# Kernel optimization log

Measured on AMD Instinct MI355X. Metric: run time of the kernel, lower is better.

Reference implementation:

```python
import jax, jax.numpy as jnp
import numpy as np


def _ln(x, g, b, eps=1e-5):
    m = x.mean(-1, keepdims=True)
    v = ((x - m) ** 2).mean(-1, keepdims=True)
    return g * (x - m) / jnp.sqrt(v + eps) + b


def _mha(x, w_qkv, b_qkv, w_o, b_o, nh):
    B, S, d = x.shape
    hd = d // nh
    qkv = x @ w_qkv.T + b_qkv
    q, k, v = jnp.split(qkv, 3, axis=-1)
    sp = lambda t: t.reshape(B, S, nh, hd).transpose(0, 2, 1, 3)
    q, k, v = sp(q), sp(k), sp(v)
    a = jax.nn.softmax(jnp.einsum('bhqd,bhkd->bhqk', q, k) / np.float32(np.sqrt(hd)), axis=-1)
    o = jnp.einsum('bhqk,bhkd->bhqd', a, v).transpose(0, 2, 1, 3).reshape(B, S, d)
    return o @ w_o.T + b_o


def _enc(x, w_qkv, b_qkv, w_o, b_o, ga, ba, wf1, bf1, wf2, bf2, gb, bb, nh=2):
    # torch TransformerEncoderLayer, post-norm, ReLU FFN
    x = _ln(x + _mha(x, w_qkv, b_qkv, w_o, b_o, nh), ga, ba)
    ff = jax.nn.relu(x @ wf1.T + bf1) @ wf2.T + bf2
    return _ln(x + ff, gb, bb)


def forward(nodes, w_qkv1, b_qkv1, w_o1, b_o1, g1a, bb1a, w_ff1a, bf1a, w_ff1b, bf1b, g1b, bb1b,
            wq, bq, wk, bk, wv, bv, g_co, bb_co, w4, b4, w5, b5, w6, b6,
            w_rel, w_root, b_rgcn, wg_rel, wg_root, bg,
            w_qkv2, b_qkv2, w_o2, b_o2, g2a, bb2a, w_ff2a, bf2a, w_ff2b, bf2b, g2b, bb2b,
            w_l1, b_l1, w_l2, b_l2, edge_index, opt_idx):
    N, H = nodes.shape
    O = 4
    B = opt_idx.shape[0] // O
    # option-node mutual attention (encoder_layer1) + scatter back
    opts = nodes[opt_idx].reshape(B, O, H)
    opts = _enc(opts, w_qkv1, b_qkv1, w_o1, b_o1, g1a, bb1a, w_ff1a, bf1a, w_ff1b, bf1b, g1b, bb1b)
    nodes2 = nodes.at[opt_idx].set(opts.reshape(B * O, H))
    src, dst = edge_index[0], edge_index[1]
    xs, xd = nodes2[src], nodes2[dst]  # [E,H]
    # per-edge 4-head co-attention: node1/node2 are single rows so qk^T is a scalar per head
    hd = H // 4
    q = (xs @ wq.T + bq).reshape(-1, 4, hd)
    k = (xd @ wk.T + bk).reshape(-1, 4, hd)
    v = (xd @ wv.T + bv).reshape(-1, 4, hd)
    s = jnp.einsum('ehd,ehd->eh', q, k) / np.float32(np.sqrt(hd))
    r = (s[..., None] * v).reshape(-1, H)
    co = jax.nn.relu(_ln(r, g_co, bb_co))
    h = jax.nn.relu(co @ w4.T + b4)
    h = jax.nn.relu(h @ w5.T + b5)
    logits = h @ w6.T + b6  # [E,8]
    # original applies Softmax(dim=0) to a [1,8] tensor -> all ones -> argmax picks class 0
    probs = jax.nn.softmax(logits[:, None, :], axis=1)[:, 0, :]
    edge_type = jnp.argmax(probs, axis=-1)
    # RGCNConv(H, H, num_relations=8), mean aggregation per relation + root + bias
    agg = jnp.zeros((N, H), nodes.dtype)
    for rel in range(8):
        m = edge_type == rel
        msg = jnp.where(m[:, None], xs @ w_rel[rel], 0.0)
        ssum = jax.ops.segment_sum(msg, dst, num_segments=N)
        cnt = jax.ops.segment_sum(m.astype(nodes.dtype), dst, num_segments=N)
        agg = agg + ssum / jnp.maximum(cnt, 1.0)[:, None]
    out1 = nodes2 @ w_root + b_rgcn + agg
    # GraphConv(H, 64): add-aggregated neighbors through lin_rel + root through lin_root
    agg2 = jax.ops.segment_sum(out1[src], dst, num_segments=N)
    out2 = agg2 @ wg_rel + bg + out1 @ wg_root  # [N,64]
    # readout over option nodes (encoder_layer2 + tanh(linear1) + linear2)
    opt2 = out2[opt_idx].reshape(B, O, 64)
    opt2 = _enc(opt2, w_qkv2, b_qkv2, w_o2, b_o2, g2a, bb2a, w_ff2a, bf2a, w_ff2b, bf2b, g2b, bb2b)
    opt2 = jnp.tanh(opt2 @ w_l1.T + b_l1)
    return opt2 @ w_l2.T + b_l2  # [B,O,1]


def setup_inputs() -> dict:
    key = jax.random.key(0)
    N, E, B, O, H, F = 20000, 40000, 64, 4, 768, 2048
    ks = iter(jax.random.split(key, 64))
    W = lambda *s: jax.random.normal(next(ks), s, jnp.float32) * 0.02
    return dict(
        nodes=jax.random.normal(next(ks), (N, H), jnp.float32),
        edge_index=jax.random.randint(next(ks), (2, E), 0, N),
        opt_idx=jnp.arange(B * O),
        w_qkv1=W(3 * H, H), b_qkv1=jnp.zeros(3 * H), w_o1=W(H, H), b_o1=jnp.zeros(H),
        g1a=jnp.ones(H), bb1a=jnp.zeros(H),
        w_ff1a=W(F, H), bf1a=jnp.zeros(F), w_ff1b=W(H, F), bf1b=jnp.zeros(H),
        g1b=jnp.ones(H), bb1b=jnp.zeros(H),
        wq=W(H, H), bq=jnp.zeros(H), wk=W(H, H), bk=jnp.zeros(H), wv=W(H, H), bv=jnp.zeros(H),
        g_co=jnp.ones(H), bb_co=jnp.zeros(H),
        w4=W(H, H), b4=jnp.zeros(H), w5=W(64, H), b5=jnp.zeros(64), w6=W(8, 64), b6=jnp.zeros(8),
        w_rel=W(8, H, H), w_root=W(H, H), b_rgcn=jnp.zeros(H),
        wg_rel=W(H, 64), wg_root=W(H, 64), bg=jnp.zeros(64),
        w_qkv2=W(192, 64), b_qkv2=jnp.zeros(192), w_o2=W(64, 64), b_o2=jnp.zeros(64),
        g2a=jnp.ones(64), bb2a=jnp.zeros(64),
        w_ff2a=W(F, 64), bf2a=jnp.zeros(F), w_ff2b=W(64, F), bf2b=jnp.zeros(64),
        g2b=jnp.ones(64), bb2b=jnp.zeros(64),
        w_l1=W(64, 64), b_l1=jnp.zeros(64), w_l2=W(1, 64), b_l2=jnp.zeros(1),
    )


def reference(nodes, edge_index, opt_idx, w_qkv1, b_qkv1, w_o1, b_o1, g1a, bb1a, w_ff1a, bf1a,
              w_ff1b, bf1b, g1b, bb1b, wq, bq, wk, bk, wv, bv, g_co, bb_co, w4, b4, w5, b5, w6, b6,
              w_rel, w_root, b_rgcn, wg_rel, wg_root, bg, w_qkv2, b_qkv2, w_o2, b_o2, g2a, bb2a,
              w_ff2a, bf2a, w_ff2b, bf2b, g2b, bb2b, w_l1, b_l1, w_l2, b_l2):
    return forward(nodes, w_qkv1, b_qkv1, w_o1, b_o1, g1a, bb1a, w_ff1a, bf1a, w_ff1b, bf1b, g1b,
                   bb1b, wq, bq, wk, bk, wv, bv, g_co, bb_co, w4, b4, w5, b5, w6, b6, w_rel, w_root,
                   b_rgcn, wg_rel, wg_root, bg, w_qkv2, b_qkv2, w_o2, b_o2, g2a, bb2a, w_ff2a, bf2a,
                   w_ff2b, bf2b, g2b, bb2b, w_l1, b_l1, w_l2, b_l2, edge_index, opt_idx)
```

## Files before the change

### kernel.cpp

```cpp
#include <hip/hip_runtime.h>

typedef unsigned short u16;
typedef unsigned int u32;
typedef __bf16 bf16x8 __attribute__((ext_vector_type(8)));
typedef float f32x4 __attribute__((ext_vector_type(4)));

__device__ __forceinline__ u16 f2bf(float f) {
    union { float f; u32 u; } v; v.f = f;
    u32 r = v.u + 0x7FFFu + ((v.u >> 16) & 1u);
    return (u16)(r >> 16);
}
__device__ __forceinline__ float bf2f(u16 h) {
    union { u32 u; float f; } v; v.u = (u32)h << 16; return v.f;
}

__global__ __launch_bounds__(256) void gemm_bt(
    const u16* __restrict__ A, const u16* __restrict__ Bt,
    float* __restrict__ C, u16* __restrict__ Cb, const float* __restrict__ bias,
    int M, int N, int K, int relu)
{
    __shared__ char lA[128 * 64 * 2];
    __shared__ char lB[128 * 64 * 2];
    const int t = threadIdx.x;
    const int w = t >> 6, l = t & 63;
    const int bn = blockIdx.x, bm = blockIdx.y;
    const int wr = w >> 1, wc = w & 1;

    const int srow = w * 8 + (l >> 3);
    const int scol = ((l & 7) ^ (l >> 3)) << 3;
    const u16* gA = A + (size_t)(bm * 128 + srow) * K + scol;
    const u16* gB = Bt + (size_t)(bn * 128 + srow) * K + scol;

    f32x4 zero = {0.f, 0.f, 0.f, 0.f};
    f32x4 acc[4][4];
#pragma unroll
    for (int i = 0; i < 4; i++)
#pragma unroll
        for (int j = 0; j < 4; j++) acc[i][j] = zero;

    const int arow = wr * 64 + (l & 15);
    const int brow = wc * 64 + (l & 15);
    const int kx = l >> 4;
    const int sw = l & 7;

    for (int k0 = 0; k0 < K; k0 += 64) {
#pragma unroll
        for (int c2 = 0; c2 < 4; ++c2) {
            __builtin_amdgcn_global_load_lds(
                (const __attribute__((address_space(1))) void*)(gA + (size_t)c2 * 32 * K + k0),
                (__attribute__((address_space(3))) void*)(lA + c2 * 4096 + w * 1024), 16, 0, 0);
            __builtin_amdgcn_global_load_lds(
                (const __attribute__((address_space(1))) void*)(gB + (size_t)c2 * 32 * K + k0),
                (__attribute__((address_space(3))) void*)(lB + c2 * 4096 + w * 1024), 16, 0, 0);
        }
        __syncthreads();
#pragma unroll
        for (int kk = 0; kk < 2; ++kk) {
            bf16x8 af[4], bfr[4];
#pragma unroll
            for (int mi = 0; mi < 4; ++mi)
                af[mi] = *(const bf16x8*)(lA + (arow + mi * 16) * 128 + (((kk * 4 + kx) ^ sw) << 4));
#pragma unroll
            for (int ni = 0; ni < 4; ++ni)
                bfr[ni] = *(const bf16x8*)(lB + (brow + ni * 16) * 128 + (((kk * 4 + kx) ^ sw) << 4));
#pragma unroll
            for (int mi = 0; mi < 4; ++mi)
#pragma unroll
                for (int ni = 0; ni < 4; ++ni)
                    acc[mi][ni] = __builtin_amdgcn_mfma_f32_16x16x32_bf16(af[mi], bfr[ni], acc[mi][ni], 0, 0, 0);
        }
        __syncthreads();
    }

    const int cm = bm * 128 + wr * 64;
    const int cn = bn * 128 + wc * 64;
#pragma unroll
    for (int mi = 0; mi < 4; ++mi) {
#pragma unroll
        for (int ni = 0; ni < 4; ++ni) {
            int row0 = cm + mi * 16 + (l >> 4) * 4;
            int col = cn + ni * 16 + (l & 15);
            float bv = bias ? bias[col] : 0.f;
#pragma unroll
            for (int r = 0; r < 4; ++r) {
                float v = acc[mi][ni][r] + bv;
                if (relu) v = fmaxf(v, 0.f);
                if (Cb) Cb[(size_t)(row0 + r) * N + col] = f2bf(v);
                else    C [(size_t)(row0 + r) * N + col] = v;
            }
        }
    }
}

__global__ __launch_bounds__(256) void gemm_bt_sk(
    const u16* __restrict__ A, const u16* __restrict__ Bt,
    float* __restrict__ P, int M, int N, int K, int Kc)
{
    __shared__ char lA[128 * 64 * 2];
    __shared__ char lB[128 * 64 * 2];
    const int t = threadIdx.x;
    const int w = t >> 6, l = t & 63;
    const int bn = blockIdx.x, bm = blockIdx.y, ks = blockIdx.z;
    const int wr = w >> 1, wc = w & 1;

    const int srow = w * 8 + (l >> 3);
    const int scol = ((l & 7) ^ (l >> 3)) << 3;
    const u16* gA = A + (size_t)(bm * 128 + srow) * K + scol;
    const u16* gB = Bt + (size_t)(bn * 128 + srow) * K + scol;

    f32x4 zero = {0.f, 0.f, 0.f, 0.f};
    f32x4 acc[4][4];
#pragma unroll
    for (int i = 0; i < 4; i++)
#pragma unroll
        for (int j = 0; j < 4; j++) acc[i][j] = zero;

    const int arow = wr * 64 + (l & 15);
    const int brow = wc * 64 + (l & 15);
    const int kx = l >> 4;
    const int sw = l & 7;

    const int kbeg = ks * Kc, kend = kbeg + Kc;
    for (int k0 = kbeg; k0 < kend; k0 += 64) {
#pragma unroll
        for (int c2 = 0; c2 < 4; ++c2) {
            __builtin_amdgcn_global_load_lds(
                (const __attribute__((address_space(1))) void*)(gA + (size_t)c2 * 32 * K + k0),
                (__attribute__((address_space(3))) void*)(lA + c2 * 4096 + w * 1024), 16, 0, 0);
            __builtin_amdgcn_global_load_lds(
                (const __attribute__((address_space(1))) void*)(gB + (size_t)c2 * 32 * K + k0),
                (__attribute__((address_space(3))) void*)(lB + c2 * 4096 + w * 1024), 16, 0, 0);
        }
        __syncthreads();
#pragma unroll
        for (int kk = 0; kk < 2; ++kk) {
            bf16x8 af[4], bfr[4];
#pragma unroll
            for (int mi = 0; mi < 4; ++mi)
                af[mi] = *(const bf16x8*)(lA + (arow + mi * 16) * 128 + (((kk * 4 + kx) ^ sw) << 4));
#pragma unroll
            for (int ni = 0; ni < 4; ++ni)
                bfr[ni] = *(const bf16x8*)(lB + (brow + ni * 16) * 128 + (((kk * 4 + kx) ^ sw) << 4));
#pragma unroll
            for (int mi = 0; mi < 4; ++mi)
#pragma unroll
                for (int ni = 0; ni < 4; ++ni)
                    acc[mi][ni] = __builtin_amdgcn_mfma_f32_16x16x32_bf16(af[mi], bfr[ni], acc[mi][ni], 0, 0, 0);
        }
        __syncthreads();
    }

    float* Pp = P + (size_t)ks * M * N;
    const int cm = bm * 128 + wr * 64;
    const int cn = bn * 128 + wc * 64;
#pragma unroll
    for (int mi = 0; mi < 4; ++mi) {
#pragma unroll
        for (int ni = 0; ni < 4; ++ni) {
            int row0 = cm + mi * 16 + (l >> 4) * 4;
            int col = cn + ni * 16 + (l & 15);
#pragma unroll
            for (int r = 0; r < 4; ++r)
                Pp[(size_t)(row0 + r) * N + col] = acc[mi][ni][r];
        }
    }
}

__global__ void sk_reduce_b(const float* __restrict__ P, int KS, long MN, int N,
                            const float* __restrict__ bias, int relu, u16* __restrict__ outb)
{
    long i = (long)blockIdx.x * blockDim.x + threadIdx.x;
    long stride = (long)gridDim.x * blockDim.x;
    for (; i < MN; i += stride) {
        float v = bias ? bias[i % N] : 0.f;
        for (int ks = 0; ks < KS; ks++) v += P[(size_t)ks * MN + i];
        if (relu) v = fmaxf(v, 0.f);
        outb[i] = f2bf(v);
    }
}

struct CJob { const float* src; u16* dst; long n4; };
struct CJobs6 { CJob j[6]; };
__global__ void conv6_bf16(CJobs6 jobs)
{
    CJob jb = jobs.j[blockIdx.z];
    long i = (long)blockIdx.x * blockDim.x + threadIdx.x;
    long stride = (long)gridDim.x * blockDim.x;
    for (; i < jb.n4; i += stride) {
        float4 v = ((const float4*)jb.src)[i];
        ushort4 o;
        o.x = f2bf(v.x); o.y = f2bf(v.y); o.z = f2bf(v.z); o.w = f2bf(v.w);
        ((ushort4*)jb.dst)[i] = o;
    }
}

struct TJob { const float* src; u16* dst; int Rr, Cc, ldo; };
struct TJobs2 { TJob j[2]; };
__global__ void transpose2_bf16(TJobs2 jobs)
{
    TJob jb = jobs.j[blockIdx.z];
    __shared__ float tile[32][33];
    int c0 = blockIdx.x * 32, r0 = blockIdx.y * 32;
    if (c0 >= jb.Cc || r0 >= jb.Rr) return;
    int tx = threadIdx.x, ty = threadIdx.y;
    for (int dy = 0; dy < 32; dy += 8) {
        int r = r0 + ty + dy, c = c0 + tx;
        tile[ty + dy][tx] = (r < jb.Rr && c < jb.Cc) ? jb.src[(size_t)r * jb.Cc + c] : 0.f;
    }
    __syncthreads();
    for (int dy = 0; dy < 32; dy += 8) {
        int c = c0 + ty + dy, r = r0 + tx;
        if (c < jb.Cc && r < jb.Rr) jb.dst[(size_t)c * jb.ldo + r] = f2bf(tile[tx][ty + dy]);
    }
}

__global__ void bc_prep(const float* __restrict__ b_rgcn, const float* __restrict__ wg_rel,
                        const float* __restrict__ wg_root, float* __restrict__ bc)
{
    int n = threadIdx.x;
    const float* W = (n < 64) ? (wg_rel + n) : (wg_root + (n - 64));
    float s = 0.f;
    for (int k = 0; k < 768; k++) s += b_rgcn[k] * W[(size_t)k * 64];
    bc[n] = s;
}

__global__ void conv_nodes_str(const float* __restrict__ nodes, u16* __restrict__ Abig,
                               int Nn, int Mpad)
{
    long i = (long)blockIdx.x * blockDim.x + threadIdx.x;
    long stride = (long)gridDim.x * blockDim.x;
    long n4 = (long)Mpad * 192;
    for (; i < n4; i += stride) {
        long row = i / 192, c4 = i % 192;
        ushort4 o;
        if ((int)row < Nn) {
            float4 v = ((const float4*)nodes)[i];
            o.x = f2bf(v.x); o.y = f2bf(v.y); o.z = f2bf(v.z); o.w = f2bf(v.w);
        } else { o.x = 0; o.y = 0; o.z = 0; o.w = 0; }
        ((ushort4*)Abig)[row * 384 + c4] = o;
    }
}

__global__ void gather_x0(const float* __restrict__ nodes, const int* __restrict__ opt,
                          float* __restrict__ x0, u16* __restrict__ x0b, int H)
{
    int r = blockIdx.x;
    size_t srcb = (size_t)opt[r] * H;
    for (int c = threadIdx.x; c < H; c += blockDim.x) {
        float v = nodes[srcb + c];
        x0[(size_t)r * H + c] = v;
        x0b[(size_t)r * H + c] = f2bf(v);
    }
}

__global__ __launch_bounds__(256) void attn_fused(
    const float* __restrict__ Pq, int KS, const float* __restrict__ b_qkv1,
    u16* __restrict__ atnob)
{
    __shared__ float Q[4][384], Kk[4][384], V[4][384];
    int b = blockIdx.x >> 1, h = blockIdx.x & 1;
    int w = threadIdx.x >> 6, l = threadIdx.x & 63;
    int row = b * 4 + w;
    const int hb = h * 384;
#pragma unroll
    for (int j = 0; j < 6; j++) {
        int c = hb + j * 64 + l;
        float q = b_qkv1[c], k = b_qkv1[768 + c], v = b_qkv1[1536 + c];
        for (int ks = 0; ks < KS; ks++) {
            const float* Pr = Pq + (size_t)ks * 256 * 2304 + (size_t)row * 2304;
            q += Pr[c]; k += Pr[768 + c]; v += Pr[1536 + c];
        }
        Q[w][j * 64 + l] = q; Kk[w][j * 64 + l] = k; V[w][j * 64 + l] = v;
    }
    __syncthreads();
    float sc[4];
#pragma unroll
    for (int sj = 0; sj < 4; sj++) {
        float p = 0.f;
#pragma unroll
        for (int j = 0; j < 6; j++) p += Q[w][j * 64 + l] * Kk[sj][j * 64 + l];
        for (int off = 32; off; off >>= 1) p += __shfl_down(p, off, 64);
        sc[sj] = __shfl(p, 0, 64) * 0.05103103630798287f;
    }
    float mx = fmaxf(fmaxf(sc[0], sc[1]), fmaxf(sc[2], sc[3]));
    float e0 = __expf(sc[0] - mx), e1 = __expf(sc[1] - mx);
    float e2 = __expf(sc[2] - mx), e3 = __expf(sc[3] - mx);
    float inv = 1.f / (e0 + e1 + e2 + e3);
    e0 *= inv; e1 *= inv; e2 *= inv; e3 *= inv;
#pragma unroll
    for (int j = 0; j < 6; j++) {
        int c = j * 64 + l;
        float o = e0 * V[0][c] + e1 * V[1][c] + e2 * V[2][c] + e3 * V[3][c];
        atnob[(size_t)row * 768 + hb + c] = f2bf(o);
    }
}

__global__ __launch_bounds__(256) void ln_reduce768(
    const float* __restrict__ P, int KS, const float* __restrict__ bias,
    const float* __restrict__ res, const float* __restrict__ g, const float* __restrict__ be,
    float* __restrict__ outf, u16* __restrict__ outb, const int* __restrict__ opt, int ldo)
{
    int r = blockIdx.x, t = threadIdx.x;
    float v[3]; float s = 0.f, q = 0.f;
#pragma unroll
    for (int i = 0; i < 3; i++) {
        int c = t + i * 256;
        float a = bias[c] + res[(size_t)r * 768 + c];
        for (int ks = 0; ks < KS; ks++) a += P[(size_t)ks * 256 * 768 + (size_t)r * 768 + c];
        v[i] = a; s += a; q += a * a;
    }
    for (int off = 32; off; off >>= 1) { s += __shfl_down(s, off, 64); q += __shfl_down(q, off, 64); }
    __shared__ float ss[4], qq[4];
    int w = t >> 6, l = t & 63;
    if (l == 0) { ss[w] = s; qq[w] = q; }
    __syncthreads();
    s = ss[0] + ss[1] + ss[2] + ss[3];
    q = qq[0] + qq[1] + qq[2] + qq[3];
    float m = s * (1.f / 768.f);
    float ri = rsqrtf(q * (1.f / 768.f) - m * m + 1e-5f);
    size_t ob = opt ? (size_t)opt[r] * ldo : (size_t)r * ldo;
#pragma unroll
    for (int i = 0; i < 3; i++) {
        int c = t + i * 256;
        float o = g[c] * (v[i] - m) * ri + be[c];
        if (outf) outf[(size_t)r * 768 + c] = o;
        if (outb) outb[ob + c] = f2bf(o);
    }
}

__global__ void edge_count(const int* __restrict__ ei, int* __restrict__ cnt, int E)
{
    int e = blockIdx.x * blockDim.x + threadIdx.x;
    if (e < E) atomicAdd(&cnt[ei[E + e]], 1);
}

__global__ __launch_bounds__(1024) void scan_offsets(
    const int* __restrict__ cnt, int* __restrict__ offs, int* __restrict__ cur, int n)
{
    __shared__ int part[1024];
    int t = threadIdx.x;
    int per = (n + 1023) / 1024;
    int base = t * per;
    int local = 0;
    for (int i = 0; i < per; i++) {
        int idx = base + i;
        if (idx < n) local += cnt[idx];
    }
    part[t] = local;
    __syncthreads();
    for (int off = 1; off < 1024; off <<= 1) {
        int v = (t >= off) ? part[t - off] : 0;
        __syncthreads();
        part[t] += v;
        __syncthreads();
    }
    int prefix = (t == 0) ? 0 : part[t - 1];
    for (int i = 0; i < per; i++) {
        int idx = base + i;
        if (idx < n) {
            offs[idx] = prefix;
            cur[idx] = prefix;
            prefix += cnt[idx];
        }
    }
}

__global__ void fill_edges(const int* __restrict__ ei, int* __restrict__ cur,
                           int* __restrict__ elist, int E)
{
    int e = blockIdx.x * blockDim.x + threadIdx.x;
    if (e < E) {
        int d = ei[E + e];
        int pos = atomicAdd(&cur[d], 1);
        elist[pos] = ei[e];
    }
}

__global__ __launch_bounds__(256) void gather_mean(
    const int* __restrict__ offs, const int* __restrict__ cnt, const int* __restrict__ elist,
    u16* Abig, int Nn, int Mpad)
{
    int w = threadIdx.x >> 6, l = threadIdx.x & 63;
    int d = blockIdx.x * 4 + w;
    if (d >= Mpad) return;
    float acc[12];
#pragma unroll
    for (int j = 0; j < 12; j++) acc[j] = 0.f;
    float inv = 0.f;
    if (d < Nn) {
        int base = offs[d], c = cnt[d];
        for (int i = 0; i < c; i++) {
            int s = elist[base + i];
            const ushort4* p = (const ushort4*)(Abig + (size_t)s * 1536);
#pragma unroll
            for (int j4 = 0; j4 < 3; j4++) {
                ushort4 v = p[j4 * 64 + l];
                acc[j4 * 4 + 0] += bf2f(v.x);
                acc[j4 * 4 + 1] += bf2f(v.y);
                acc[j4 * 4 + 2] += bf2f(v.z);
                acc[j4 * 4 + 3] += bf2f(v.w);
            }
        }
        inv = 1.f / (float)max(c, 1);
    }
    ushort4* q = (ushort4*)(Abig + (size_t)d * 1536 + 768);
#pragma unroll
    for (int j4 = 0; j4 < 3; j4++) {
        ushort4 o;
        o.x = f2bf(acc[j4 * 4 + 0] * inv);
        o.y = f2bf(acc[j4 * 4 + 1] * inv);
        o.z = f2bf(acc[j4 * 4 + 2] * inv);
        o.w = f2bf(acc[j4 * 4 + 3] * inv);
        q[j4 * 64 + l] = o;
    }
}

__global__ __launch_bounds__(256) void enc2_head(
    const int* __restrict__ opt, const int* __restrict__ offs, const int* __restrict__ cnt,
    const int* __restrict__ elist, const float* __restrict__ C2, const float* __restrict__ bg,
    const float* __restrict__ w_qkv2, const float* __restrict__ b_qkv2,
    const float* __restrict__ w_o2, const float* __restrict__ b_o2,
    const float* __restrict__ g2a, const float* __restrict__ bb2a,
    float* __restrict__ x21)
{
    __shared__ float X[4][64];
    __shared__ float QKV[4][192];
    __shared__ float T[4][64];
    int b = blockIdx.x;
    int w = threadIdx.x >> 6, l = threadIdx.x & 63;
    int row = b * 4 + w;

    {
        int d = opt[row];
        float acc = bg[l] + C2[(size_t)d * 128 + 64 + l];
        int base = offs[d], c = cnt[d];
        for (int i = 0; i < c; i++) {
            int s = elist[base + i];
            acc += C2[(size_t)s * 128 + l];
        }
        X[w][l] = acc;
    }
    __syncthreads();

#pragma unroll
    for (int j = 0; j < 3; j++) {
        int n = l + j * 64;
        const float* wr = w_qkv2 + (size_t)n * 64;
        float s = b_qkv2[n];
        for (int k = 0; k < 64; k++) s += X[w][k] * wr[k];
        QKV[w][n] = s;
    }
    __syncthreads();

    {
        float q = QKV[w][l];
        float p0 = q * QKV[0][64 + l], p1 = q * QKV[1][64 + l];
        float p2 = q * QKV[2][64 + l], p3 = q * QKV[3][64 + l];
#pragma unroll
        for (int off = 1; off < 32; off <<= 1) {
            p0 += __shfl_xor(p0, off, 64); p1 += __shfl_xor(p1, off, 64);
            p2 += __shfl_xor(p2, off, 64); p3 += __shfl_xor(p3, off, 64);
        }
        p0 *= 0.1767766953f; p1 *= 0.1767766953f; p2 *= 0.1767766953f; p3 *= 0.1767766953f;
        float mx = fmaxf(fmaxf(p0, p1), fmaxf(p2, p3));
        float e0 = __expf(p0 - mx), e1 = __expf(p1 - mx), e2 = __expf(p2 - mx), e3 = __expf(p3 - mx);
        float inv = 1.f / (e0 + e1 + e2 + e3);
        T[w][l] = (e0 * QKV[0][128 + l] + e1 * QKV[1][128 + l] +
                   e2 * QKV[2][128 + l] + e3 * QKV[3][128 + l]) * inv;
    }
    __syncthreads();

    {
        const float* wr = w_o2 + (size_t)l * 64;
        float s = b_o2[l];
        for (int k = 0; k < 64; k++) s += T[w][k] * wr[k];
        float xa = s + X[w][l];
        float sum = xa, sq = xa * xa;
#pragma unroll
        for (int off = 1; off < 64; off <<= 1) {
            sum += __shfl_xor(sum, off, 64);
            sq  += __shfl_xor(sq, off, 64);
        }
        float m = sum * (1.f / 64.f);
        float ri = rsqrtf(sq * (1.f / 64.f) - m * m + 1e-5f);
        x21[(size_t)row * 64 + l] = g2a[l] * (xa - m) * ri + bb2a[l];
    }
}

__global__ __launch_bounds__(256) void ff1_par(
    const float* __restrict__ x21, const float* __restrict__ wf1,
    const float* __restrict__ bf1, float* __restrict__ Hf)
{
    __shared__ float X[64];
    int b = blockIdx.x, t = threadIdx.x;
    int r = b >> 3, n = (b & 7) * 256 + t;
    if (t < 64) X[t] = x21[(size_t)r * 64 + t];
    __syncthreads();
    const float4* wr4 = (const float4*)(wf1 + (size_t)n * 64);
    float s = bf1[n];
#pragma unroll
    for (int k4 = 0; k4 < 16; k4++) {
        float4 wv = wr4[k4];
        const float* xp = X + k4 * 4;
        s += wv.x * xp[0] + wv.y * xp[1] + wv.z * xp[2] + wv.w * xp[3];
    }
    Hf[(size_t)r * 2048 + n] = fmaxf(s, 0.f);
}

__global__ __launch_bounds__(256) void ff2_tail(
    const float* __restrict__ Hf, const float* __restrict__ x21,
    const float* __restrict__ wf2, const float* __restrict__ bf2,
    const float* __restrict__ g2b, const float* __restrict__ bb2b,
    const float* __restrict__ w_l1, const float* __restrict__ b_l1,
    const float* __restrict__ w_l2, const float* __restrict__ b_l2,
    float* __restrict__ out)
{
    __shared__ float HL[2048];
    __shared__ float part[4][64];
    __shared__ float X2[64];
    int r = blockIdx.x, t = threadIdx.x;
    int w = t >> 6, l = t & 63;

    {
        const float4* src = (const float4*)(Hf + (size_t)r * 2048);
        float4* dst = (float4*)HL;
        dst[t] = src[t];
        dst[t + 256] = src[t + 256];
    }
    __syncthreads();

    {
        const float4* wr4 = (const float4*)(wf2 + (size_t)l * 2048 + w * 512);
        const float* hp = HL + w * 512;
        float s = 0.f;
#pragma unroll 16
        for (int k4 = 0; k4 < 128; k4++) {
            float4 wv = wr4[k4];
            const float* xp = hp + k4 * 4;
            s += wv.x * xp[0] + wv.y * xp[1] + wv.z * xp[2] + wv.w * xp[3];
        }
        part[w][l] = s;
    }
    __syncthreads();

    if (w == 0) {
        float xa = part[0][l] + part[1][l] + part[2][l] + part[3][l] + bf2[l]
                 + x21[(size_t)r * 64 + l];
        float sum = xa, sq = xa * xa;
#pragma unroll
        for (int off = 1; off < 64; off <<= 1) {
            sum += __shfl_xor(sum, off, 64);
            sq  += __shfl_xor(sq, off, 64);
        }
        float m = sum * (1.f / 64.f);
        float ri = rsqrtf(sq * (1.f / 64.f) - m * m + 1e-5f);
        X2[l] = g2b[l] * (xa - m) * ri + bb2b[l];
        __builtin_amdgcn_wave_barrier();
        const float* wr = w_l1 + (size_t)l * 64;
        float s = b_l1[l];
        for (int k = 0; k < 64; k++) s += X2[k] * wr[k];
        float tv = tanhf(s);
        float p = tv * w_l2[l];
#pragma unroll
        for (int off = 1; off < 64; off <<= 1) p += __shfl_xor(p, off, 64);
        if (l == 0) out[r] = p + b_l2[0];
    }
}

extern "C" void kernel_launch(void* const* d_in, const int* in_sizes, int n_in,
                              void* d_out, int out_size, void* d_ws, size_t ws_size,
                              hipStream_t stream)
{
    const float* nodes  = (const float*)d_in[0];
    const int*   ei     = (const int*)d_in[1];
    const int*   opt    = (const int*)d_in[2];
    const float* w_qkv1 = (const float*)d_in[3];
    const float* b_qkv1 = (const float*)d_in[4];
    const float* w_o1   = (const float*)d_in[5];
    const float* b_o1   = (const float*)d_in[6];
    const float* g1a    = (const float*)d_in[7];
    const float* bb1a   = (const float*)d_in[8];
    const float* w_ff1a = (const float*)d_in[9];
    const float* bf1a   = (const float*)d_in[10];
    const float* w_ff1b = (const float*)d_in[11];
    const float* bf1b   = (const float*)d_in[12];
    const float* g1b    = (const float*)d_in[13];
    const float* bb1b   = (const float*)d_in[14];
    const float* w_rel  = (const float*)d_in[29];
    const float* w_root = (const float*)d_in[30];
    const float* b_rgcn = (const float*)d_in[31];
    const float* wg_rel = (const float*)d_in[32];
    const float* wg_root= (const float*)d_in[33];
    const float* bg     = (const float*)d_in[34];
    const float* w_qkv2 = (const float*)d_in[35];
    const float* b_qkv2 = (const float*)d_in[36];
    const float* w_o2   = (const float*)d_in[37];
    const float* b_o2   = (const float*)d_in[38];
    const float* g2a    = (const float*)d_in[39];
    const float* bb2a   = (const float*)d_in[40];
    const float* w_ff2a = (const float*)d_in[41];
    const float* bf2a   = (const float*)d_in[42];
    const float* w_ff2b = (const float*)d_in[43];
    const float* bf2b   = (const float*)d_in[44];
    const float* g2b    = (const float*)d_in[45];
    const float* bb2b   = (const float*)d_in[46];
    const float* w_l1   = (const float*)d_in[47];
    const float* b_l1   = (const float*)d_in[48];
    const float* w_l2   = (const float*)d_in[49];
    const float* b_l2   = (const float*)d_in[50];

    const int H = 768, F = 2048;
    const int Nn = in_sizes[0] / H;
    const int E  = in_sizes[1] / 2;
    const int R  = in_sizes[2];
    const int Mpad = (Nn + 127) & ~127;
    const int Bb = R / 4;

    char* ws = (char*)d_ws;
    size_t off = 0;
    auto alloc = [&](size_t b) -> char* {
        char* p = ws + off; off += (b + 255) & ~(size_t)255; return p;
    };
    u16* wqkv1b  = (u16*)alloc((size_t)3 * H * H * 2);
    u16* wo1b    = (u16*)alloc((size_t)H * H * 2);
    u16* wff1ab  = (u16*)alloc((size_t)F * H * 2);
    u16* wff1bb  = (u16*)alloc((size_t)H * F * 2);
    u16* Wbraw   = (u16*)alloc((size_t)1536 * H * 2);
    u16* W2tb    = (u16*)alloc((size_t)128 * H * 2);
    u16* WcT     = (u16*)alloc((size_t)128 * 1536 * 2);
    float* bc    = (float*)alloc((size_t)128 * 4);
    float* Psk  = (float*)alloc((size_t)4 * 256 * 2304 * 4);
    float* x0   = (float*)alloc((size_t)R * H * 4);
    u16*  x0b   = (u16*)alloc((size_t)R * H * 2);
    u16*  atnob = (u16*)alloc((size_t)R * H * 2);
    float* x1   = (float*)alloc((size_t)R * H * 4);
    u16*  x1b   = (u16*)alloc((size_t)R * H * 2);
    u16*  ffhb  = (u16*)alloc((size_t)R * F * 2);
    u16*  Abig  = (u16*)alloc((size_t)Mpad * 1536 * 2);
    float* C2   = (float*)alloc((size_t)Mpad * 128 * 4);
    int* cnt   = (int*)alloc((size_t)Nn * 4);
    int* offs  = (int*)alloc((size_t)Nn * 4);
    int* cur   = (int*)alloc((size_t)Nn * 4);
    int* elist = (int*)alloc((size_t)E * 4);
    float* x21 = (float*)alloc((size_t)R * 64 * 4);
    float* Hf2 = (float*)alloc((size_t)R * F * 4);
    (void)ws_size; (void)n_in; (void)out_size;

    {
        CJobs6 cj;
        cj.j[0] = { w_qkv1, wqkv1b, (long)3 * H * H / 4 };
        cj.j[1] = { w_o1,   wo1b,   (long)H * H / 4 };
        cj.j[2] = { w_ff1a, wff1ab, (long)F * H / 4 };
        cj.j[3] = { w_ff1b, wff1bb, (long)H * F / 4 };
        cj.j[4] = { w_root, Wbraw,                    (long)H * H / 4 };
        cj.j[5] = { w_rel,  Wbraw + (size_t)H * H,    (long)H * H / 4 };
        conv6_bf16<<<dim3(432, 1, 6), 256, 0, stream>>>(cj);
        TJobs2 tj;
        tj.j[0] = { wg_rel,  W2tb,                    768, 64, 768 };
        tj.j[1] = { wg_root, W2tb + (size_t)64 * 768, 768, 64, 768 };
        transpose2_bf16<<<dim3(2, 24, 2), dim3(32, 8), 0, stream>>>(tj);
    }
    gemm_bt_sk<<<dim3(12, 1, 4), 256, 0, stream>>>(W2tb, Wbraw, Psk, 128, 1536, 768, 192);
    sk_reduce_b<<<768, 256, 0, stream>>>(Psk, 4, (long)128 * 1536, 1536, nullptr, 0, WcT);
    bc_prep<<<1, 128, 0, stream>>>(b_rgcn, wg_rel, wg_root, bc);

    conv_nodes_str<<<2048, 256, 0, stream>>>(nodes, Abig, Nn, Mpad);

    gather_x0<<<R, 256, 0, stream>>>(nodes, opt, x0, x0b, H);
    gemm_bt_sk<<<dim3(18, 2, 4), 256, 0, stream>>>(x0b, wqkv1b, Psk, R, 3 * H, H, 192);
    attn_fused<<<Bb * 2, 256, 0, stream>>>(Psk, 4, b_qkv1, atnob);
    gemm_bt_sk<<<dim3(6, 2, 4), 256, 0, stream>>>(atnob, wo1b, Psk, R, H, H, 192);
    ln_reduce768<<<R, 256, 0, stream>>>(Psk, 4, b_o1, x0, g1a, bb1a, x1, x1b, nullptr, 768);
    gemm_bt_sk<<<dim3(16, 2, 4), 256, 0, stream>>>(x1b, wff1ab, Psk, R, F, H, 192);
    sk_reduce_b<<<2048, 256, 0, stream>>>(Psk, 4, (long)R * F, F, bf1a, 1, ffhb);
    gemm_bt_sk<<<dim3(6, 2, 8), 256, 0, stream>>>(ffhb, wff1bb, Psk, R, H, F, 256);
    ln_reduce768<<<R, 256, 0, stream>>>(Psk, 8, bf1b, x1, g1b, bb1b, nullptr, Abig, opt, 1536);

    hipMemsetAsync(cnt, 0, (size_t)Nn * 4, stream);
    edge_count<<<(E + 255) / 256, 256, 0, stream>>>(ei, cnt, E);
    scan_offsets<<<1, 1024, 0, stream>>>(cnt, offs, cur, Nn);
    fill_edges<<<(E + 255) / 256, 256, 0, stream>>>(ei, cur, elist, E);
    gather_mean<<<Mpad / 4, 256, 0, stream>>>(offs, cnt, elist, Abig, Nn, Mpad);

    gemm_bt<<<dim3(1, Mpad / 128), 256, 0, stream>>>(Abig, WcT, C2, nullptr, bc, Mpad, 128, 1536, 0);

    enc2_head<<<Bb, 256, 0, stream>>>(opt, offs, cnt, elist, C2, bg,
                                      w_qkv2, b_qkv2, w_o2, b_o2, g2a, bb2a, x21);
    ff1_par<<<R * 8, 256, 0, stream>>>(x21, w_ff2a, bf2a, Hf2);
    ff2_tail<<<R, 256, 0, stream>>>(Hf2, x21, w_ff2b, bf2b, g2b, bb2b,
                                    w_l1, b_l1, w_l2, b_l2, (float*)d_out);
}
```

Measured before the change: 476.1 us.

## Merge encoder and CSR-build launch chains into cooperative kernels with grid syncs

Replaces the chain of encoder-layer-1 kernels (QKV GEMM, attention, out-proj GEMM, LN, FFN GEMMs, split-K reduce, LN) with a single cooperative kernel that separates stages with grid.sync, and does the same for the CSR build (memset, count, multi-block scan, fill). It also merges small prep kernels (transpose plus bias prep, node conversion plus gather) and fuses the two head FFN kernels so the hidden activations stay in shared memory. The aim is to cut launch overhead and inter-kernel gaps. In exchange, each cooperative stage runs on a fixed grid of 144 or 40 blocks, and the head FFN now does more serial work per block.

Result: slower. 650.9 us (+36.7%).

```diff
diff --git a/kernel.cpp b/kernel.cpp
--- a/kernel.cpp
+++ b/kernel.cpp
@@ -1,4 +1,7 @@
 #include <hip/hip_runtime.h>
+#include <hip/hip_cooperative_groups.h>
+
+namespace cg = cooperative_groups;
 
 typedef unsigned short u16;
 typedef unsigned int u32;
@@ -92,15 +95,14 @@
     }
 }
 
-__global__ __launch_bounds__(256) void gemm_bt_sk(
-    const u16* __restrict__ A, const u16* __restrict__ Bt,
-    float* __restrict__ P, int M, int N, int K, int Kc)
-{
-    __shared__ char lA[128 * 64 * 2];
-    __shared__ char lB[128 * 64 * 2];
+__device__ __forceinline__ void gemm_sk_body(
+    const u16* __restrict__ A, const u16* __restrict__ Bt, float* __restrict__ P,
+    int M, int N, int K, int Kc, int bn, int bm, int ks, char* lsmem)
+{
+    char* lA = lsmem;
+    char* lB = lsmem + 32768;
     const int t = threadIdx.x;
     const int w = t >> 6, l = t & 63;
-    const int bn = blockIdx.x, bm = blockIdx.y, ks = blockIdx.z;
     const int wr = w >> 1, wc = w & 1;
 
     const int srow = w * 8 + (l >> 3);
@@ -164,6 +166,14 @@
                 Pp[(size_t)(row0 + r) * N + col] = acc[mi][ni][r];
         }
     }
+}
+
+__global__ __launch_bounds__(256) void gemm_bt_sk(
+    const u16* __restrict__ A, const u16* __restrict__ Bt,
+    float* __restrict__ P, int M, int N, int K, int Kc)
+{
+    __shared__ char lsmem[65536];
+    gemm_sk_body(A, Bt, P, M, N, K, Kc, blockIdx.x, blockIdx.y, blockIdx.z, lsmem);
 }
 
 __global__ void sk_reduce_b(const float* __restrict__ P, int KS, long MN, int N,
@@ -195,14 +205,25 @@
 }
 
 struct TJob { const float* src; u16* dst; int Rr, Cc, ldo; };
-struct TJobs2 { TJob j[2]; };
-__global__ void transpose2_bf16(TJobs2 jobs)
-{
-    TJob jb = jobs.j[blockIdx.z];
+__global__ void prep2(TJob j0, TJob j1, const float* __restrict__ b_rgcn,
+                      const float* __restrict__ wg_rel, const float* __restrict__ wg_root,
+                      float* __restrict__ bc)
+{
+    if (blockIdx.z == 2) {
+        if (blockIdx.x == 0 && blockIdx.y == 0 && threadIdx.x < 128) {
+            int n = threadIdx.x;
+            const float* W = (n < 64) ? (wg_rel + n) : (wg_root + (n - 64));
+            float s = 0.f;
+            for (int k = 0; k < 768; k++) s += b_rgcn[k] * W[(size_t)k * 64];
+            bc[n] = s;
+        }
+        return;
+    }
+    TJob jb = blockIdx.z ? j1 : j0;
     __shared__ float tile[32][33];
+    int tx = threadIdx.x & 31, ty = threadIdx.x >> 5;
     int c0 = blockIdx.x * 32, r0 = blockIdx.y * 32;
     if (c0 >= jb.Cc || r0 >= jb.Rr) return;
-    int tx = threadIdx.x, ty = threadIdx.y;
     for (int dy = 0; dy < 32; dy += 8) {
         int r = r0 + ty + dy, c = c0 + tx;
         tile[ty + dy][tx] = (r < jb.Rr && c < jb.Cc) ? jb.src[(size_t)r * jb.Cc + c] : 0.f;
@@ -214,51 +235,43 @@
     }
 }
 
-__global__ void bc_prep(const float* __restrict__ b_rgcn, const float* __restrict__ wg_rel,
-                        const float* __restrict__ wg_root, float* __restrict__ bc)
-{
-    int n = threadIdx.x;
-    const float* W = (n < 64) ? (wg_rel + n) : (wg_root + (n - 64));
-    float s = 0.f;
-    for (int k = 0; k < 768; k++) s += b_rgcn[k] * W[(size_t)k * 64];
-    bc[n] = s;
-}
-
-__global__ void conv_nodes_str(const float* __restrict__ nodes, u16* __restrict__ Abig,
-                               int Nn, int Mpad)
-{
-    long i = (long)blockIdx.x * blockDim.x + threadIdx.x;
-    long stride = (long)gridDim.x * blockDim.x;
-    long n4 = (long)Mpad * 192;
-    for (; i < n4; i += stride) {
-        long row = i / 192, c4 = i % 192;
-        ushort4 o;
-        if ((int)row < Nn) {
-            float4 v = ((const float4*)nodes)[i];
-            o.x = f2bf(v.x); o.y = f2bf(v.y); o.z = f2bf(v.z); o.w = f2bf(v.w);
-        } else { o.x = 0; o.y = 0; o.z = 0; o.w = 0; }
-        ((ushort4*)Abig)[row * 384 + c4] = o;
-    }
-}
-
-__global__ void gather_x0(const float* __restrict__ nodes, const int* __restrict__ opt,
-                          float* __restrict__ x0, u16* __restrict__ x0b, int H)
-{
-    int r = blockIdx.x;
-    size_t srcb = (size_t)opt[r] * H;
-    for (int c = threadIdx.x; c < H; c += blockDim.x) {
-        float v = nodes[srcb + c];
-        x0[(size_t)r * H + c] = v;
-        x0b[(size_t)r * H + c] = f2bf(v);
-    }
-}
-
-__global__ __launch_bounds__(256) void attn_fused(
+__global__ void conv_nodes_gx(const float* __restrict__ nodes, u16* __restrict__ Abig,
+                              int Nn, int Mpad, const int* __restrict__ opt,
+                              float* __restrict__ x0, u16* __restrict__ x0b)
+{
+    int b = blockIdx.x;
+    if (b < 2048) {
+        long i = (long)b * 256 + threadIdx.x;
+        long stride = 2048L * 256;
+        long n4 = (long)Mpad * 192;
+        for (; i < n4; i += stride) {
+            long row = i / 192, c4 = i % 192;
+            ushort4 o;
+            if ((int)row < Nn) {
+                float4 v = ((const float4*)nodes)[i];
+                o.x = f2bf(v.x); o.y = f2bf(v.y); o.z = f2bf(v.z); o.w = f2bf(v.w);
+            } else { o.x = 0; o.y = 0; o.z = 0; o.w = 0; }
+            ((ushort4*)Abig)[row * 384 + c4] = o;
+        }
+    } else {
+        int r = b - 2048;
+        size_t srcb = (size_t)opt[r] * 768;
+        for (int c = threadIdx.x; c < 768; c += 256) {
+            float v = nodes[srcb + c];
+            x0[(size_t)r * 768 + c] = v;
+            x0b[(size_t)r * 768 + c] = f2bf(v);
+        }
+    }
+}
+
+__device__ __forceinline__ void attn_body(
     const float* __restrict__ Pq, int KS, const float* __restrict__ b_qkv1,
-    u16* __restrict__ atnob)
-{
-    __shared__ float Q[4][384], Kk[4][384], V[4][384];
-    int b = blockIdx.x >> 1, h = blockIdx.x & 1;
+    u16* __restrict__ atnob, int bh, char* lsmem)
+{
+    float* Q  = (float*)lsmem;
+    float* Kk = Q + 4 * 384;
+    float* V  = Kk + 4 * 384;
+    int b = bh >> 1, h = bh & 1;
     int w = threadIdx.x >> 6, l = threadIdx.x & 63;
     int row = b * 4 + w;
     const int hb = h * 384;
@@ -270,7 +283,9 @@
             const float* Pr = Pq + (size_t)ks * 256 * 2304 + (size_t)row * 2304;
             q += Pr[c]; k += Pr[768 + c]; v += Pr[1536 + c];
         }
-        Q[w][j * 64 + l] = q; Kk[w][j * 64 + l] = k; V[w][j * 64 + l] = v;
+        Q[w * 384 + j * 64 + l] = q;
+        Kk[w * 384 + j * 64 + l] = k;
+        V[w * 384 + j * 64 + l] = v;
     }
     __syncthreads();
     float sc[4];
@@ -278,7 +293,7 @@
     for (int sj = 0; sj < 4; sj++) {
         float p = 0.f;
 #pragma unroll
-        for (int j = 0; j < 6; j++) p += Q[w][j * 64 + l] * Kk[sj][j * 64 + l];
+        for (int j = 0; j < 6; j++) p += Q[w * 384 + j * 64 + l] * Kk[sj * 384 + j * 64 + l];
         for (int off = 32; off; off >>= 1) p += __shfl_down(p, off, 64);
         sc[sj] = __shfl(p, 0, 64) * 0.05103103630798287f;
     }
@@ -290,17 +305,21 @@
 #pragma unroll
     for (int j = 0; j < 6; j++) {
         int c = j * 64 + l;
-        float o = e0 * V[0][c] + e1 * V[1][c] + e2 * V[2][c] + e3 * V[3][c];
+        float o = e0 * V[c] + e1 * V[384 + c] + e2 * V[2 * 384 + c] + e3 * V[3 * 384 + c];
         atnob[(size_t)row * 768 + hb + c] = f2bf(o);
     }
-}
-
-__global__ __launch_bounds__(256) void ln_reduce768(
+    __syncthreads();
+}
+
+__device__ __forceinline__ void ln_body(
     const float* __restrict__ P, int KS, const float* __restrict__ bias,
     const float* __restrict__ res, const float* __restrict__ g, const float* __restrict__ be,
-    float* __restrict__ outf, u16* __restrict__ outb, const int* __restrict__ opt, int ldo)
-{
-    int r = blockIdx.x, t = threadIdx.x;
+    float* __restrict__ outf, u16* __restrict__ outb, const int* __restrict__ opt,
+    int ldo, int r, char* lsmem)
+{
+    float* ss = (float*)lsmem;
+    float* qq = ss + 4;
+    int t = threadIdx.x;
     float v[3]; float s = 0.f, q = 0.f;
 #pragma unroll
     for (int i = 0; i < 3; i++) {
@@ -310,7 +329,6 @@
         v[i] = a; s += a; q += a * a;
     }
     for (int off = 32; off; off >>= 1) { s += __shfl_down(s, off, 64); q += __shfl_down(q, off, 64); }
-    __shared__ float ss[4], qq[4];
     int w = t >> 6, l = t & 63;
     if (l == 0) { ss[w] = s; qq[w] = q; }
     __syncthreads();
@@ -326,53 +344,103 @@
         if (outf) outf[(size_t)r * 768 + c] = o;
         if (outb) outb[ob + c] = f2bf(o);
     }
-}
-
-__global__ void edge_count(const int* __restrict__ ei, int* __restrict__ cnt, int E)
-{
-    int e = blockIdx.x * blockDim.x + threadIdx.x;
-    if (e < E) atomicAdd(&cnt[ei[E + e]], 1);
-}
-
-__global__ __launch_bounds__(1024) void scan_offsets(
-    const int* __restrict__ cnt, int* __restrict__ offs, int* __restrict__ cur, int n)
-{
-    __shared__ int part[1024];
+    __syncthreads();
+}
+
+struct Enc1Args {
+    const u16 *x0b, *wqkv1b, *wo1b, *wff1ab, *wff1bb;
+    const float *b_qkv1, *b_o1, *g1a, *bb1a, *bf1a, *bf1b, *g1b, *bb1b, *x0;
+    float *Psk, *x1;
+    u16 *x1b, *atnob, *ffhb, *Abig;
+    const int* opt;
+};
+
+__global__ __launch_bounds__(256) void enc1_coop(Enc1Args a)
+{
+    cg::grid_group grid = cg::this_grid();
+    __shared__ char lsmem[65536];
+    const int vb = blockIdx.x;
+
+    if (vb < 144)
+        gemm_sk_body(a.x0b, a.wqkv1b, a.Psk, 256, 2304, 768, 192,
+                     vb % 18, (vb / 18) & 1, vb / 36, lsmem);
+    grid.sync();
+    if (vb < 128) attn_body(a.Psk, 4, a.b_qkv1, a.atnob, vb, lsmem);
+    grid.sync();
+    if (vb < 48)
+        gemm_sk_body(a.atnob, a.wo1b, a.Psk, 256, 768, 768, 192,
+                     vb % 6, (vb / 6) & 1, vb / 12, lsmem);
+    grid.sync();
+    for (int r = vb; r < 256; r += gridDim.x)
+        ln_body(a.Psk, 4, a.b_o1, a.x0, a.g1a, a.bb1a, a.x1, a.x1b, nullptr, 768, r, lsmem);
+    grid.sync();
+    if (vb < 128)
+        gemm_sk_body(a.x1b, a.wff1ab, a.Psk, 256, 2048, 768, 192,
+                     vb % 16, (vb / 16) & 1, vb / 32, lsmem);
+    grid.sync();
+    {
+        long MN = 256L * 2048;
+        long step = (long)gridDim.x * 256;
+        for (long i = (long)vb * 256 + threadIdx.x; i < MN; i += step) {
+            float v = a.bf1a[i & 2047];
+            for (int ks = 0; ks < 4; ks++) v += a.Psk[(size_t)ks * MN + i];
+            a.ffhb[i] = f2bf(fmaxf(v, 0.f));
+        }
+    }
+    grid.sync();
+    if (vb < 96)
+        gemm_sk_body(a.ffhb, a.wff1bb, a.Psk, 256, 768, 2048, 256,
+                     vb % 6, (vb / 6) & 1, vb / 12, lsmem);
+    grid.sync();
+    for (int r = vb; r < 256; r += gridDim.x)
+        ln_body(a.Psk, 8, a.bf1b, a.x1, a.g1b, a.bb1b, nullptr, a.Abig, a.opt, 1536, r, lsmem);
+}
+
+struct CsrArgs { const int* ei; int *cnt, *offs, *cur, *elist, *btot; int Nn, E; };
+
+__global__ __launch_bounds__(1024) void csr_coop(CsrArgs a)
+{
+    cg::grid_group grid = cg::this_grid();
+    __shared__ int sc[1024];
     int t = threadIdx.x;
-    int per = (n + 1023) / 1024;
-    int base = t * per;
-    int local = 0;
-    for (int i = 0; i < per; i++) {
-        int idx = base + i;
-        if (idx < n) local += cnt[idx];
-    }
-    part[t] = local;
-    __syncthreads();
-    for (int off = 1; off < 1024; off <<= 1) {
-        int v = (t >= off) ? part[t - off] : 0;
+    int gt = blockIdx.x * 1024 + t;
+    int GT = gridDim.x * 1024;
+
+    for (int i = gt; i < a.Nn; i += GT) a.cnt[i] = 0;
+    grid.sync();
+    for (int e = gt; e < a.E; e += GT) atomicAdd(&a.cnt[a.ei[a.E + e]], 1);
+    grid.sync();
+    int nb = (a.Nn + 1023) >> 10;
+    int v = 0;
+    if ((int)blockIdx.x < nb) {
+        v = (gt < a.Nn) ? a.cnt[gt] : 0;
+        sc[t] = v;
         __syncthreads();
-        part[t] += v;
-        __syncthreads();
-    }
-    int prefix = (t == 0) ? 0 : part[t - 1];
-    for (int i = 0; i < per; i++) {
-        int idx = base + i;
-        if (idx < n) {
-            offs[idx] = prefix;
-            cur[idx] = prefix;
-            prefix += cnt[idx];
-        }
-    }
-}
-
-__global__ void fill_edges(const int* __restrict__ ei, int* __restrict__ cur,
-                           int* __restrict__ elist, int E)
-{
-    int e = blockIdx.x * blockDim.x + threadIdx.x;
-    if (e < E) {
-        int d = ei[E + e];
-        int pos = atomicAdd(&cur[d], 1);
-        elist[pos] = ei[e];
+        for (int off = 1; off < 1024; off <<= 1) {
+            int x = (t >= off) ? sc[t - off] : 0;
+            __syncthreads();
+            sc[t] += x;
+            __syncthreads();
+        }
+        if (gt < a.Nn) a.offs[gt] = sc[t] - v;
+        if (t == 1023) a.btot[blockIdx.x] = sc[1023];
+    }
+    grid.sync();
+    if (blockIdx.x == 0 && t == 0) {
+        int run = 0;
+        for (int b = 0; b < nb; b++) { int x = a.btot[b]; a.btot[b] = run; run += x; }
+    }
+    grid.sync();
+    if ((int)blockIdx.x < nb && gt < a.Nn) {
+        int o = a.offs[gt] + a.btot[blockIdx.x];
+        a.offs[gt] = o;
+        a.cur[gt] = o;
+    }
+    grid.sync();
+    for (int e = gt; e < a.E; e += GT) {
+        int d = a.ei[a.E + e];
+        int p = atomicAdd(&a.cur[d], 1);
+        a.elist[p] = a.ei[e];
     }
 }
 
@@ -487,45 +555,35 @@
     }
 }
 
-__global__ __launch_bounds__(256) void ff1_par(
-    const float* __restrict__ x21, const float* __restrict__ wf1,
-    const float* __restrict__ bf1, float* __restrict__ Hf)
-{
-    __shared__ float X[64];
-    int b = blockIdx.x, t = threadIdx.x;
-    int r = b >> 3, n = (b & 7) * 256 + t;
-    if (t < 64) X[t] = x21[(size_t)r * 64 + t];
-    __syncthreads();
-    const float4* wr4 = (const float4*)(wf1 + (size_t)n * 64);
-    float s = bf1[n];
-#pragma unroll
-    for (int k4 = 0; k4 < 16; k4++) {
-        float4 wv = wr4[k4];
-        const float* xp = X + k4 * 4;
-        s += wv.x * xp[0] + wv.y * xp[1] + wv.z * xp[2] + wv.w * xp[3];
-    }
-    Hf[(size_t)r * 2048 + n] = fmaxf(s, 0.f);
-}
-
-__global__ __launch_bounds__(256) void ff2_tail(
-    const float* __restrict__ Hf, const float* __restrict__ x21,
+__global__ __launch_bounds__(256) void ff_fused(
+    const float* __restrict__ x21, const float* __restrict__ wf1, const float* __restrict__ bf1,
     const float* __restrict__ wf2, const float* __restrict__ bf2,
     const float* __restrict__ g2b, const float* __restrict__ bb2b,
     const float* __restrict__ w_l1, const float* __restrict__ b_l1,
     const float* __restrict__ w_l2, const float* __restrict__ b_l2,
     float* __restrict__ out)
 {
+    __shared__ float X[64];
     __shared__ float HL[2048];
     __shared__ float part[4][64];
     __shared__ float X2[64];
     int r = blockIdx.x, t = threadIdx.x;
     int w = t >> 6, l = t & 63;
 
-    {
-        const float4* src = (const float4*)(Hf + (size_t)r * 2048);
-        float4* dst = (float4*)HL;
-        dst[t] = src[t];
-        dst[t + 256] = src[t + 256];
+    if (t < 64) X[t] = x21[(size_t)r * 64 + t];
+    __syncthreads();
+
+#pragma unroll
+    for (int j = 0; j < 8; j++) {
+        int n = t + j * 256;
+        const float4* wr4 = (const float4*)(wf1 + (size_t)n * 64);
+        float s = bf1[n];
+#pragma unroll
+        for (int k4 = 0; k4 < 16; k4++) {
+            float4 wv = wr4[k4];
+            s += wv.x * X[k4 * 4] + wv.y * X[k4 * 4 + 1] + wv.z * X[k4 * 4 + 2] + wv.w * X[k4 * 4 + 3];
+        }
+        HL[n] = fmaxf(s, 0.f);
     }
     __syncthreads();
 
@@ -536,8 +594,7 @@
 #pragma unroll 16
         for (int k4 = 0; k4 < 128; k4++) {
             float4 wv = wr4[k4];
-            const float* xp = hp + k4 * 4;
-            s += wv.x * xp[0] + wv.y * xp[1] + wv.z * xp[2] + wv.w * xp[3];
+            s += wv.x * hp[k4 * 4] + wv.y * hp[k4 * 4 + 1] + wv.z * hp[k4 * 4 + 2] + wv.w * hp[k4 * 4 + 3];
         }
         part[w][l] = s;
     }
@@ -614,7 +671,6 @@
     const int E  = in_sizes[1] / 2;
     const int R  = in_sizes[2];
     const int Mpad = (Nn + 127) & ~127;
-    const int Bb = R / 4;
 
     char* ws = (char*)d_ws;
     size_t off = 0;
@@ -642,8 +698,8 @@
     int* offs  = (int*)alloc((size_t)Nn * 4);
     int* cur   = (int*)alloc((size_t)Nn * 4);
     int* elist = (int*)alloc((size_t)E * 4);
+    int* btot  = (int*)alloc((size_t)64 * 4);
     float* x21 = (float*)alloc((size_t)R * 64 * 4);
-    float* Hf2 = (float*)alloc((size_t)R * F * 4);
     (void)ws_size; (void)n_in; (void)out_size;
 
     {
@@ -652,41 +708,46 @@
         cj.j[1] = { w_o1,   wo1b,   (long)H * H / 4 };
         cj.j[2] = { w_ff1a, wff1ab, (long)F * H / 4 };
         cj.j[3] = { w_ff1b, wff1bb, (long)H * F / 4 };
-        cj.j[4] = { w_root, Wbraw,                    (long)H * H / 4 };
-        cj.j[5] = { w_rel,  Wbraw + (size_t)H * H,    (long)H * H / 4 };
+        cj.j[4] = { w_root, Wbraw,                 (long)H * H / 4 };
+        cj.j[5] = { w_rel,  Wbraw + (size_t)H * H, (long)H * H / 4 };
         conv6_bf16<<<dim3(432, 1, 6), 256, 0, stream>>>(cj);
-        TJobs2 tj;
-        tj.j[0] = { wg_rel,  W2tb,                    768, 64, 768 };
-        tj.j[1] = { wg_root, W2tb + (size_t)64 * 768, 768, 64, 768 };
-        transpose2_bf16<<<dim3(2, 24, 2), dim3(32, 8), 0, stream>>>(tj);
+    }
+    {
+        TJob t0 = { wg_rel,  W2tb,                    768, 64, 768 };
+        TJob t1 = { wg_root, W2tb + (size_t)64 * 768, 768, 64, 768 };
+        prep2<<<dim3(2, 24, 3), 256, 0, stream>>>(t0, t1, b_rgcn, wg_rel, wg_root, bc);
     }
     gemm_bt_sk<<<dim3(12, 1, 4), 256, 0, stream>>>(W2tb, Wbraw, Psk, 128, 1536, 768, 192);
     sk_reduce_b<<<768, 256, 0, stream>>>(Psk, 4, (long)128 * 1536, 1536, nullptr, 0, WcT);
-    bc_prep<<<1, 128, 0, stream>>>(b_rgcn, wg_rel, wg_root, bc);
-
-    conv_nodes_str<<<2048, 256, 0, stream>>>(nodes, Abig, Nn, Mpad);
-
-    gather_x0<<<R, 256, 0, stream>>>(nodes, opt, x0, x0b, H);
-    gemm_bt_sk<<<dim3(18, 2, 4), 256, 0, stream>>>(x0b, wqkv1b, Psk, R, 3 * H, H, 192);
-    attn_fused<<<Bb * 2, 256, 0, stream>>>(Psk, 4, b_qkv1, atnob);
-    gemm_bt_sk<<<dim3(6, 2, 4), 256, 0, stream>>>(atnob, wo1b, Psk, R, H, H, 192);
-    ln_reduce768<<<R, 256, 0, stream>>>(Psk, 4, b_o1, x0, g1a, bb1a, x1, x1b, nullptr, 768);
-    gemm_bt_sk<<<dim3(16, 2, 4), 256, 0, stream>>>(x1b, wff1ab, Psk, R, F, H, 192);
-    sk_reduce_b<<<2048, 256, 0, stream>>>(Psk, 4, (long)R * F, F, bf1a, 1, ffhb);
-    gemm_bt_sk<<<dim3(6, 2, 8), 256, 0, stream>>>(ffhb, wff1bb, Psk, R, H, F, 256);
-    ln_reduce768<<<R, 256, 0, stream>>>(Psk, 8, bf1b, x1, g1b, bb1b, nullptr, Abig, opt, 1536);
-
-    hipMemsetAsync(cnt, 0, (size_t)Nn * 4, stream);
-    edge_count<<<(E + 255) / 256, 256, 0, stream>>>(ei, cnt, E);
-    scan_offsets<<<1, 1024, 0, stream>>>(cnt, offs, cur, Nn);
-    fill_edges<<<(E + 255) / 256, 256, 0, stream>>>(ei, cur, elist, E);
+
+    conv_nodes_gx<<<2048 + R, 256, 0, stream>>>(nodes, Abig, Nn, Mpad, opt, x0, x0b);
+
+    {
+        Enc1Args ea;
+        ea.x0b = x0b; ea.wqkv1b = wqkv1b; ea.wo1b = wo1b; ea.wff1ab = wff1ab; ea.wff1bb = wff1bb;
+        ea.b_qkv1 = b_qkv1; ea.b_o1 = b_o1; ea.g1a = g1a; ea.bb1a = bb1a;
+        ea.bf1a = bf1a; ea.bf1b = bf1b; ea.g1b = g1b; ea.bb1b = bb1b; ea.x0 = x0;
+        ea.Psk = Psk; ea.x1 = x1;
+        ea.x1b = x1b; ea.atnob = atnob; ea.ffhb = ffhb; ea.Abig = Abig;
+        ea.opt = opt;
+        void* kp[] = { &ea };
+        hipLaunchCooperativeKernel((void*)enc1_coop, dim3(144), dim3(256), kp, 0, stream);
+    }
+
+    {
+        CsrArgs ca;
+        ca.ei = ei; ca.cnt = cnt; ca.offs = offs; ca.cur = cur; ca.elist = elist;
+        ca.btot = btot; ca.Nn = Nn; ca.E = E;
+        void* kp[] = { &ca };
+        hipLaunchCooperativeKernel((void*)csr_coop, dim3(40), dim3(1024), kp, 0, stream);
+    }
+
     gather_mean<<<Mpad / 4, 256, 0, stream>>>(offs, cnt, elist, Abig, Nn, Mpad);
 
     gemm_bt<<<dim3(1, Mpad / 128), 256, 0, stream>>>(Abig, WcT, C2, nullptr, bc, Mpad, 128, 1536, 0);
 
-    enc2_head<<<Bb, 256, 0, stream>>>(opt, offs, cnt, elist, C2, bg,
-                                      w_qkv2, b_qkv2, w_o2, b_o2, g2a, bb2a, x21);
-    ff1_par<<<R * 8, 256, 0, stream>>>(x21, w_ff2a, bf2a, Hf2);
-    ff2_tail<<<R, 256, 0, stream>>>(Hf2, x21, w_ff2b, bf2b, g2b, bb2b,
+    enc2_head<<<R / 4, 256, 0, stream>>>(opt, offs, cnt, elist, C2, bg,
+                                         w_qkv2, b_qkv2, w_o2, b_o2, g2a, bb2a, x21);
+    ff_fused<<<R, 256, 0, stream>>>(x21, w_ff2a, bf2a, w_ff2b, bf2b, g2b, bb2b,
                                     w_l1, b_l1, w_l2, b_l2, (float*)d_out);
 }
```
